# Performance work log

Hardware: AMD Instinct MI355X
Metric: run time of the kernel (lower is better)

The kernel has to match this reference:

```python
import jax, jax.numpy as jnp
import numpy as np

M_FIELDS = 26   # cin_size[0]
H1 = 128        # cin_size[1]
H2 = 128        # cin_size[2]
BATCH = 2048
EMB_K = 32


def setup_inputs() -> dict:
    key = jax.random.key(0)
    k0, k1, k2, k3, k4 = jax.random.split(key, 5)
    inputs = jax.random.normal(k0, (BATCH, M_FIELDS, EMB_K), dtype=jnp.float32)
    # Conv3d(1, H1, kernel=(26,26,1)) -> weight [H1, H_prev=26, m=26], bias [H1]
    W1 = jax.random.normal(k1, (H1, M_FIELDS, M_FIELDS), dtype=jnp.float32) * 0.05
    b1 = jax.random.normal(k2, (H1,), dtype=jnp.float32) * 0.05
    # Conv3d(1, H2, kernel=(H1,26,1)) -> weight [H2, H1, m=26], bias [H2]
    W2 = jax.random.normal(k3, (H2, H1, M_FIELDS), dtype=jnp.float32) * 0.05
    b2 = jax.random.normal(k4, (H2,), dtype=jnp.float32) * 0.05
    return {"inputs": inputs, "W1": W1, "b1": b1, "W2": W2, "b2": b2}


def _cin_layer(x_prev, x0, W, b):
    # x_prev: [B, H_prev, k], x0: [B, m, k], W: [H, H_prev, m], b: [H]
    # Equivalent to: outer product z[b,i,j,k] = x_prev[b,i,k]*x0[b,j,k],
    # then Conv3d with kernel (H_prev, m, 1): out[b,h,k] = sum_ij W[h,i,j]*z + b[h]
    return jnp.einsum('bik,bjk,hij->bhk', x_prev, x0, W) + b[None, :, None]


def reference(inputs, W1, b1, W2, b2):
    x1 = _cin_layer(inputs, inputs, W1, b1)   # [B, H1, k]
    x2 = _cin_layer(x1, inputs, W2, b2)       # [B, H2, k]
    res = jnp.concatenate([x1, x2], axis=1)   # [B, H1+H2, k]
    return jnp.sum(res, axis=-1)              # [B, H1+H2]
```

## Files before the change

kernel.cpp:

```cpp
#include <hip/hip_runtime.h>

typedef __bf16 bf16;
typedef __bf16 bf16x8 __attribute__((ext_vector_type(8)));
typedef __bf16 bf16x4 __attribute__((ext_vector_type(4)));
typedef float f32x4 __attribute__((ext_vector_type(4)));
typedef unsigned int u32;

#define NB    2048
#define NM    26
#define NJP   27

__global__ __launch_bounds__(256) void prep_all(
    const float* __restrict__ W1, const float* __restrict__ W2,
    bf16* __restrict__ w1t, bf16* __restrict__ w2t2)
{
  const int bid = blockIdx.x, t = threadIdx.x;
  #pragma unroll
  for (int g = 0; g < 4; ++g) {
    int ge = g*160768 + bid*256 + t;
    if (ge < 110592) {
      int e = ge;
      int el = e & 7, lr = (e >> 3) & 15, lq = (e >> 7) & 3, ni = (e >> 9) & 3;
      int rest = e >> 11;
      int c = rest % NJP, cs_idx = rest / NJP;
      int h = cs_idx*64 + ni*16 + lr;
      int i = lq*8 + el;
      float v = (i < NM && c < NM) ? W1[h*(NM*NM) + i*NM + c] : 0.f;
      w1t[e] = (bf16)v;
    } else {
      int e = ge - 110592;
      int el = e & 7, lr = (e >> 3) & 15, lq = (e >> 7) & 3, ni = (e >> 9) & 3;
      int rest = e >> 11;
      int kc = rest % 130, cs_idx = rest / 130;
      int h = cs_idx*64 + ni*16 + lr;
      int c = lq*8 + el;
      float v = (kc < 128 && c < NM) ? W2[h*(128*NM) + kc*NM + c] : 0.f;
      w2t2[e] = (bf16)v;
    }
  }
}

#define STEP(CUR, NXT, J) do {                                                 \
  { int jn = ((J)+1 > 25) ? 25 : (J)+1;         \
    scf[NXT][0][0] = spw0[jn*32];  scf[NXT][0][1] = spw0[jn*32 + 16];          \
    scf[NXT][1][0] = spw1[jn*32];  scf[NXT][1][1] = spw1[jn*32 + 16]; }        \
  _Pragma("unroll")                                                            \
  for (int ni = 0; ni < 4; ++ni)                                               \
    B[NXT][ni] = *(const bf16x8*)(tb + (long)((J)+1)*2048 + ni*512);           \
  _Pragma("unroll")                                                            \
  for (int bb = 0; bb < 2; ++bb)                                               \
    _Pragma("unroll")                                                          \
    for (int mi = 0; mi < 2; ++mi) {                                           \
      bf16x8 af;                                                               \
      _Pragma("unroll")                                                        \
      for (int e = 0; e < 8; ++e)                                              \
        af[e] = (bf16)(xf32[bb][mi][e] * scf[CUR][bb][mi]);                    \
      _Pragma("unroll")                                                        \
      for (int ni = 0; ni < 4; ++ni)                                           \
        acc[bb][mi][ni] = __builtin_amdgcn_mfma_f32_16x16x32_bf16(af,          \
                                    B[CUR][ni], acc[bb][mi][ni], 0, 0, 0);     \
    }                                                                          \
} while (0)

__global__ __launch_bounds__(256, 2) void cin1G(
    const float* __restrict__ in, const bf16* __restrict__ w1t,
    const float* __restrict__ b1, bf16* __restrict__ G2, float* __restrict__ out)
{
  __shared__ __align__(16) bf16 ldsT[4][64*36];
  const int t = threadIdx.x, bid = blockIdx.x;
  const int lane = t & 63, w = t >> 6;
  const int lr = lane & 15, lq = lane >> 4;
  const int fo = lq*128 + lr*8;
  const int cs_idx = bid & 1, cs = cs_idx * 64;
  const int strip8 = bid >> 1;
  const int bw0 = strip8*8 + w*2;

  const float* bin0 = in + (long)bw0*(NM*32);
  const float* bin1 = bin0 + NM*32;
  const float* spw0 = bin0 + lr;
  const float* spw1 = bin1 + lr;

  float xf32[2][2][8];
  #pragma unroll
  for (int bb = 0; bb < 2; ++bb) {
    const float* bin = bb ? bin1 : bin0;
    #pragma unroll
    for (int mi = 0; mi < 2; ++mi)
      #pragma unroll
      for (int e = 0; e < 8; ++e) {
        int j = lq*8 + e;
        xf32[bb][mi][e] = (j < NM) ? bin[j*32 + mi*16 + lr] : 0.f;
      }
  }

  f32x4 acc[2][2][4];
  #pragma unroll
  for (int bb=0; bb<2; ++bb)
    #pragma unroll
    for (int mi=0; mi<2; ++mi)
      #pragma unroll
      for (int ni=0; ni<4; ++ni) acc[bb][mi][ni] = {0.f,0.f,0.f,0.f};

  const bf16* tb = w1t + (long)cs_idx*NJP*2048 + fo;

  float scf[2][2][2];
  bf16x8 B[2][4];
  #pragma unroll
  for (int ni = 0; ni < 4; ++ni)
    B[0][ni] = *(const bf16x8*)(tb + ni*512);
  scf[0][0][0] = spw0[0];  scf[0][0][1] = spw0[16];
  scf[0][1][0] = spw1[0];  scf[0][1][1] = spw1[16];

  for (int jj = 0; jj < 13; ++jj) {
    STEP(0, 1, 2*jj);
    STEP(1, 0, 2*jj + 1);
  }

  float bias[4];
  #pragma unroll
  for (int ni=0; ni<4; ++ni) bias[ni] = b1[cs + ni*16 + lr];

  bf16* T = &ldsT[w][0];

  #pragma unroll
  for (int bb = 0; bb < 2; ++bb) {
    const int bw = bw0 + bb;
    const float* bin = bb ? bin1 : bin0;

    #pragma unroll
    for (int ni=0; ni<4; ++ni) {
      float vv = 0.f;
      #pragma unroll
      for (int mi=0; mi<2; ++mi)
        #pragma unroll
        for (int r=0; r<4; ++r) vv += acc[bb][mi][ni][r];
      vv += __shfl_xor(vv, 16, 64);
      vv += __shfl_xor(vv, 32, 64);
      if (lq == 0) out[bw*256 + cs + ni*16 + lr] = vv + 32.0f * bias[ni];
    }

    #pragma unroll
    for (int mi=0; mi<2; ++mi)
      #pragma unroll
      for (int ni=0; ni<4; ++ni) {
        bf16x4 pk;
        #pragma unroll
        for (int r=0; r<4; ++r) pk[r] = (bf16)(acc[bb][mi][ni][r] + bias[ni]);
        *(bf16x4*)&T[(ni*16+lr)*36 + mi*16 + lq*4] = pk;
      }

    bf16x8 bg[2];
    #pragma unroll
    for (int nt = 0; nt < 2; ++nt) {
      int j = nt*16 + lr;
      bf16x8 vv;
      #pragma unroll
      for (int e=0; e<8; ++e) vv[e] = (bf16)0.f;
      if (j < NM) {
        const float* src = bin + j*32 + lq*8;
        f32x4 a = *(const f32x4*)src, c = *(const f32x4*)(src+4);
        #pragma unroll
        for (int e=0; e<4; ++e) { vv[e] = (bf16)a[e]; vv[4+e] = (bf16)c[e]; }
      }
      bg[nt] = vv;
    }
    const long gbase = (long)(bw >> 5)*131072 + (bw & 31)*8;
    #pragma unroll
    for (int mt = 0; mt < 4; ++mt) {
      bf16x8 ag = *(const bf16x8*)&T[(mt*16+lr)*36 + lq*8];
      #pragma unroll
      for (int nt = 0; nt < 2; ++nt) {
        f32x4 z = {0.f,0.f,0.f,0.f};
        f32x4 g = __builtin_amdgcn_mfma_f32_16x16x32_bf16(bg[nt], ag, z, 0, 0, 0);
        bf16x4 pk;
        #pragma unroll
        for (int r = 0; r < 4; ++r) pk[r] = (bf16)g[r];
        const int kh = (cs + mt*16 + lr)*4 + nt*2 + (lq >> 1);
        *(bf16x4*)&G2[gbase + (long)kh*256 + (lq & 1)*4] = pk;
      }
    }
  }
}

#define STEPG(CUR, NXT, KN) do {                                               \
  _Pragma("unroll")                                                            \
  for (int mi = 0; mi < 2; ++mi)                                               \
    A[NXT][mi] = *(const bf16x8*)(Ab + (long)(KN)*1024 + mi*128);              \
  _Pragma("unroll")                                                            \
  for (int ni = 0; ni < 4; ++ni)                                               \
    B[NXT][ni] = *(const bf16x8*)(tbc + (long)(KN)*2048 + ni*512);             \
  _Pragma("unroll")                                                            \
  for (int mi = 0; mi < 2; ++mi)                                               \
    _Pragma("unroll")                                                          \
    for (int ni = 0; ni < 4; ++ni)                                             \
      acc[mi][ni] = __builtin_amdgcn_mfma_f32_16x16x32_bf16(A[CUR][mi],        \
                                  B[CUR][ni], acc[mi][ni], 0, 0, 0);           \
} while (0)

__global__ __launch_bounds__(256, 4) void gemm2(
    const bf16* __restrict__ G2, const bf16* __restrict__ w2t2,
    const float* __restrict__ b2, float* __restrict__ out)
{
  const int t = threadIdx.x;
  const int lane = t & 63, w = t >> 6;
  const int s = blockIdx.x >> 5;
  const int q32 = blockIdx.x & 31;
  const int x = q32 & 7, q = q32 >> 3;
  const int ms = x + q*16 + (w >> 1)*8;
  const int cs_idx = w & 1;
  const int lr = lane & 15, lq = lane >> 4;
  const int fo = lq*128 + lr*8;
  const int kc0 = s*8;

  const bf16* Ab  = G2 + ((long)(ms*512 + lq)*32 + lr)*8;
  const bf16* tbc = w2t2 + (long)cs_idx*130*2048 + fo;

  f32x4 acc[2][4];
  #pragma unroll
  for (int mi=0; mi<2; ++mi)
    #pragma unroll
    for (int ni=0; ni<4; ++ni) acc[mi][ni] = {0.f,0.f,0.f,0.f};

  bf16x8 A[2][2], B[2][4];
  #pragma unroll
  for (int mi=0; mi<2; ++mi)
    A[0][mi] = *(const bf16x8*)(Ab + (long)kc0*1024 + mi*128);
  #pragma unroll
  for (int ni=0; ni<4; ++ni)
    B[0][ni] = *(const bf16x8*)(tbc + (long)kc0*2048 + ni*512);

  for (int jj = 0; jj < 4; ++jj) {
    STEPG(0, 1, kc0 + 2*jj + 1);
    STEPG(1, 0, kc0 + 2*jj + 2);
  }

  if (s == 0) {
    #pragma unroll
    for (int ni=0; ni<4; ++ni) {
      float bv = 32.0f * b2[cs_idx*64 + ni*16 + lr];
      #pragma unroll
      for (int mi=0; mi<2; ++mi)
        #pragma unroll
        for (int r=0; r<4; ++r) acc[mi][ni][r] += bv;
    }
  }

  #pragma unroll
  for (int mi=0; mi<2; ++mi)
    #pragma unroll
    for (int ni=0; ni<4; ++ni) {
      int h = cs_idx*64 + ni*16 + lr;
      #pragma unroll
      for (int r=0; r<4; ++r) {
        int b = ms*32 + mi*16 + lq*4 + r;
        atomicAdd(&out[b*256 + 128 + h], acc[mi][ni][r]);
      }
    }
}

extern "C" void kernel_launch(void* const* d_in, const int* in_sizes, int n_in,
                              void* d_out, int out_size, void* d_ws, size_t ws_size,
                              hipStream_t stream) {
  const float* in = (const float*)d_in[0];
  const float* W1 = (const float*)d_in[1];
  const float* b1 = (const float*)d_in[2];
  const float* W2 = (const float*)d_in[3];
  const float* b2 = (const float*)d_in[4];
  float* out = (float*)d_out;

  char* ws = (char*)d_ws;
  bf16* w1t  = (bf16*)(ws);
  bf16* w2t2 = (bf16*)(ws + 1048576);
  bf16* G2   = (bf16*)(ws + 4194304);

  prep_all<<<628, 256, 0, stream>>>(W1, W2, w1t, w2t2);
  cin1G  <<<512, 256, 0, stream>>>(in, w1t, b1, G2, out);
  gemm2  <<<512, 256, 0, stream>>>(G2, w2t2, b2, out);
}
```

Baseline: 111.4 us.

## Stage W2 into LDS inside gemm2 and drop its prep pass

Each gemm2 block now converts its 16-chunk slice of W2 from fp32 to bf16 directly into shared memory, instead of reading a pre-transposed global copy made by prep_all. prep_all now only handles W1. The gemm2 tiling is reshaped: each wave computes a 16-row M tile over a 16-chunk K range, with B fragments read from LDS, and occupancy is lowered to 2 blocks per SM. This removes the W2 prep writes and the global B-fragment loads, but it repeats the W2 conversion in every block and uses a smaller per-wave tile.

```diff
diff --git a/kernel.cpp b/kernel.cpp
--- a/kernel.cpp
+++ b/kernel.cpp
@@ -11,33 +11,16 @@
 #define NJP   27
 
 __global__ __launch_bounds__(256) void prep_all(
-    const float* __restrict__ W1, const float* __restrict__ W2,
-    bf16* __restrict__ w1t, bf16* __restrict__ w2t2)
+    const float* __restrict__ W1, bf16* __restrict__ w1t)
 {
-  const int bid = blockIdx.x, t = threadIdx.x;
-  #pragma unroll
-  for (int g = 0; g < 4; ++g) {
-    int ge = g*160768 + bid*256 + t;
-    if (ge < 110592) {
-      int e = ge;
-      int el = e & 7, lr = (e >> 3) & 15, lq = (e >> 7) & 3, ni = (e >> 9) & 3;
-      int rest = e >> 11;
-      int c = rest % NJP, cs_idx = rest / NJP;
-      int h = cs_idx*64 + ni*16 + lr;
-      int i = lq*8 + el;
-      float v = (i < NM && c < NM) ? W1[h*(NM*NM) + i*NM + c] : 0.f;
-      w1t[e] = (bf16)v;
-    } else {
-      int e = ge - 110592;
-      int el = e & 7, lr = (e >> 3) & 15, lq = (e >> 7) & 3, ni = (e >> 9) & 3;
-      int rest = e >> 11;
-      int kc = rest % 130, cs_idx = rest / 130;
-      int h = cs_idx*64 + ni*16 + lr;
-      int c = lq*8 + el;
-      float v = (kc < 128 && c < NM) ? W2[h*(128*NM) + kc*NM + c] : 0.f;
-      w2t2[e] = (bf16)v;
-    }
-  }
+  int e = blockIdx.x*256 + threadIdx.x;
+  int el = e & 7, lr = (e >> 3) & 15, lq = (e >> 7) & 3, ni = (e >> 9) & 3;
+  int rest = e >> 11;
+  int c = rest % NJP, cs_idx = rest / NJP;
+  int h = cs_idx*64 + ni*16 + lr;
+  int i = lq*8 + el;
+  float v = (i < NM && c < NM) ? W1[h*(NM*NM) + i*NM + c] : 0.f;
+  w1t[e] = (bf16)v;
 }
 
 #define STEP(CUR, NXT, J) do {                                                 \
@@ -182,80 +165,84 @@
   }
 }
 
-#define STEPG(CUR, NXT, KN) do {                                               \
+#define STEPG(CUR, NXT, KREL) do {                                             \
+  A[NXT] = *(const bf16x8*)(Ab + (long)(kc0 + (KREL) + 1)*1024);               \
   _Pragma("unroll")                                                            \
-  for (int mi = 0; mi < 2; ++mi)                                               \
-    A[NXT][mi] = *(const bf16x8*)(Ab + (long)(KN)*1024 + mi*128);              \
-  _Pragma("unroll")                                                            \
-  for (int ni = 0; ni < 4; ++ni)                                               \
-    B[NXT][ni] = *(const bf16x8*)(tbc + (long)(KN)*2048 + ni*512);             \
-  _Pragma("unroll")                                                            \
-  for (int mi = 0; mi < 2; ++mi)                                               \
-    _Pragma("unroll")                                                          \
-    for (int ni = 0; ni < 4; ++ni)                                             \
-      acc[mi][ni] = __builtin_amdgcn_mfma_f32_16x16x32_bf16(A[CUR][mi],        \
-                                  B[CUR][ni], acc[mi][ni], 0, 0, 0);           \
+  for (int ni = 0; ni < 4; ++ni) {                                             \
+    bf16x8 bfr = *(const bf16x8*)&ldsW[(KREL)*2048 + ni*512 + fo];             \
+    acc[ni] = __builtin_amdgcn_mfma_f32_16x16x32_bf16(A[CUR], bfr,             \
+                                                      acc[ni], 0, 0, 0);       \
+  }                                                                            \
 } while (0)
 
-__global__ __launch_bounds__(256, 4) void gemm2(
-    const bf16* __restrict__ G2, const bf16* __restrict__ w2t2,
+__global__ __launch_bounds__(256, 2) void gemm2(
+    const bf16* __restrict__ G2, const float* __restrict__ W2,
     const float* __restrict__ b2, float* __restrict__ out)
 {
-  const int t = threadIdx.x;
+  __shared__ __align__(16) bf16 ldsW[16*2048];
+  const int t = threadIdx.x, bid = blockIdx.x;
   const int lane = t & 63, w = t >> 6;
-  const int s = blockIdx.x >> 5;
-  const int q32 = blockIdx.x & 31;
-  const int x = q32 & 7, q = q32 >> 3;
-  const int ms = x + q*16 + (w >> 1)*8;
-  const int cs_idx = w & 1;
   const int lr = lane & 15, lq = lane >> 4;
   const int fo = lq*128 + lr*8;
-  const int kc0 = s*8;
-
-  const bf16* Ab  = G2 + ((long)(ms*512 + lq)*32 + lr)*8;
-  const bf16* tbc = w2t2 + (long)cs_idx*130*2048 + fo;
-
-  f32x4 acc[2][4];
-  #pragma unroll
-  for (int mi=0; mi<2; ++mi)
-    #pragma unroll
-    for (int ni=0; ni<4; ++ni) acc[mi][ni] = {0.f,0.f,0.f,0.f};
-
-  bf16x8 A[2][2], B[2][4];
-  #pragma unroll
-  for (int mi=0; mi<2; ++mi)
-    A[0][mi] = *(const bf16x8*)(Ab + (long)kc0*1024 + mi*128);
-  #pragma unroll
-  for (int ni=0; ni<4; ++ni)
-    B[0][ni] = *(const bf16x8*)(tbc + (long)kc0*2048 + ni*512);
-
-  for (int jj = 0; jj < 4; ++jj) {
-    STEPG(0, 1, kc0 + 2*jj + 1);
-    STEPG(1, 0, kc0 + 2*jj + 2);
+  const int s = bid & 7;
+  const int csx = (bid >> 3) & 1;
+  const int g = bid >> 4;
+  const int ms16 = g*4 + w;
+  const int ms32 = ms16 >> 1, mif = ms16 & 1;
+  const int kc0 = s*16;
+
+  #pragma unroll
+  for (int r = 0; r < 4; ++r) {
+    int task = r*256 + t;
+    int kcrel = task >> 6, hl = task & 63;
+    int h = csx*64 + hl, kc = kc0 + kcrel;
+    const float* src = W2 + ((long)h*128 + kc)*NM;
+    int dstb = kcrel*2048 + (hl >> 4)*512 + (hl & 15)*8;
+    #pragma unroll
+    for (int cq = 0; cq < 4; ++cq) {
+      bf16x8 pk;
+      #pragma unroll
+      for (int el = 0; el < 8; ++el) {
+        int c = cq*8 + el;
+        pk[el] = (c < NM) ? (bf16)src[c] : (bf16)0.f;
+      }
+      *(bf16x8*)&ldsW[dstb + cq*128] = pk;
+    }
+  }
+  __syncthreads();
+
+  const bf16* Ab = G2 + (long)ms32*131072 + mif*128 + lq*256 + lr*8;
+
+  f32x4 acc[4];
+  #pragma unroll
+  for (int ni=0; ni<4; ++ni) acc[ni] = {0.f,0.f,0.f,0.f};
+
+  bf16x8 A[2];
+  A[0] = *(const bf16x8*)(Ab + (long)kc0*1024);
+
+  for (int jj = 0; jj < 8; ++jj) {
+    STEPG(0, 1, 2*jj);
+    STEPG(1, 0, 2*jj + 1);
   }
 
   if (s == 0) {
     #pragma unroll
     for (int ni=0; ni<4; ++ni) {
-      float bv = 32.0f * b2[cs_idx*64 + ni*16 + lr];
-      #pragma unroll
-      for (int mi=0; mi<2; ++mi)
-        #pragma unroll
-        for (int r=0; r<4; ++r) acc[mi][ni][r] += bv;
-    }
-  }
-
-  #pragma unroll
-  for (int mi=0; mi<2; ++mi)
-    #pragma unroll
-    for (int ni=0; ni<4; ++ni) {
-      int h = cs_idx*64 + ni*16 + lr;
-      #pragma unroll
-      for (int r=0; r<4; ++r) {
-        int b = ms*32 + mi*16 + lq*4 + r;
-        atomicAdd(&out[b*256 + 128 + h], acc[mi][ni][r]);
-      }
-    }
+      float bv = 32.0f * b2[csx*64 + ni*16 + lr];
+      #pragma unroll
+      for (int r=0; r<4; ++r) acc[ni][r] += bv;
+    }
+  }
+
+  #pragma unroll
+  for (int ni=0; ni<4; ++ni) {
+    int h = csx*64 + ni*16 + lr;
+    #pragma unroll
+    for (int r=0; r<4; ++r) {
+      int b = ms16*16 + lq*4 + r;
+      atomicAdd(&out[b*256 + 128 + h], acc[ni][r]);
+    }
+  }
 }
 
 extern "C" void kernel_launch(void* const* d_in, const int* in_sizes, int n_in,
@@ -269,11 +256,10 @@
   float* out = (float*)d_out;
 
   char* ws = (char*)d_ws;
-  bf16* w1t  = (bf16*)(ws);
-  bf16* w2t2 = (bf16*)(ws + 1048576);
-  bf16* G2   = (bf16*)(ws + 4194304);
-
-  prep_all<<<628, 256, 0, stream>>>(W1, W2, w1t, w2t2);
+  bf16* w1t = (bf16*)(ws);
+  bf16* G2  = (bf16*)(ws + 4194304);
+
+  prep_all<<<432, 256, 0, stream>>>(W1, w1t);
   cin1G  <<<512, 256, 0, stream>>>(in, w1t, b1, G2, out);
-  gemm2  <<<512, 256, 0, stream>>>(G2, w2t2, b2, out);
-}
+  gemm2  <<<512, 256, 0, stream>>>(G2, W2, b2, out);
+}
```

After: 105.7 us. 1.05x faster.
